# Kernel optimization log

Hardware: AMD Instinct MI355X
Metric: run time of the kernel (lower is better)

Reference implementation:

```python
import jax, jax.numpy as jnp
import numpy as np

WS = 8          # window_size
NH = 8          # num_heads
DIM = 512
INNER = 512
CDIM = 128
CINNER = 128
SHIFTED = True
EPS = 1e-6
N = WS * WS     # tokens per window
SCALE = 1.0 / np.sqrt(INNER // NH + CINNER // NH)  # SDPA scale over fused (feat+coord) head dim


def _rmsnorm(x, g):
    return x * jax.lax.rsqrt(jnp.mean(x * x, axis=-1, keepdims=True) + EPS) * g


def _rel_indices():
    idx = np.array([[x, y] for x in range(WS) for y in range(WS)])
    ri = idx[None, :, :] - idx[:, None, :] + WS - 1
    return ri[..., 0], ri[..., 1]


def _shift_mask(Wh, Ww):
    s = WS
    k = s * (s // 2)
    row = np.zeros((N, N), np.float32)
    row[-k:, :-k] = -np.inf
    row[:-k, -k:] = -np.inf
    col = row.reshape(s, s, s, s).transpose(1, 0, 3, 2).reshape(N, N)
    m = np.zeros((Wh, Ww, N, N), np.float32)
    m[:, -1] += row
    m[-1, :] += col
    return jnp.asarray(m)


def setup_inputs() -> dict:
    key = jax.random.key(0)
    ks = jax.random.split(key, 16)
    B, h, w = 4, 128, 128

    def lin(k, fan_in, fan_out):
        return jax.random.normal(k, (fan_in, fan_out), jnp.float32) * (fan_in ** -0.5)

    return {
        "features": jax.random.normal(ks[0], (B, h, w, DIM), jnp.float32),
        "coords": jax.random.normal(ks[1], (B, h, w, CDIM), jnp.float32),
        "w_fqk": lin(ks[2], DIM, 2 * INNER),
        "b_fqk": jnp.zeros((2 * INNER,), jnp.float32),
        "g_fqk": jnp.ones((2 * INNER,), jnp.float32),
        "w_cqk": lin(ks[3], CDIM, 2 * CINNER),
        "b_cqk": jnp.zeros((2 * CINNER,), jnp.float32),
        "g_cqk": jnp.ones((2 * CINNER,), jnp.float32),
        "w_v": lin(ks[4], DIM, INNER),
        "b_v": jnp.zeros((INNER,), jnp.float32),
        "w_out": lin(ks[5], INNER, DIM),
        "b_out": jnp.zeros((DIM,), jnp.float32),
        "pos_emb": jax.random.normal(ks[6], (2 * WS - 1, 2 * WS - 1), jnp.float32),
    }


def reference(features, coords, w_fqk, b_fqk, g_fqk, w_cqk, b_cqk, g_cqk,
              w_v, b_v, w_out, b_out, pos_emb):
    B, h, w, _ = features.shape
    pad_h = (WS - h % WS) % WS
    pad_w = (WS - w % WS) % WS
    H_pad, W_pad = h + pad_h, w + pad_w
    Wh, Ww = H_pad // WS, W_pad // WS

    fqk = _rmsnorm(features @ w_fqk + b_fqk, g_fqk)
    f_q, f_k = jnp.split(fqk, 2, axis=-1)
    cqk = _rmsnorm(coords @ w_cqk + b_cqk, g_cqk)
    c_q, c_k = jnp.split(cqk, 2, axis=-1)
    f_v = features @ w_v + b_v

    def win(t):
        t = jnp.pad(t, ((0, 0), (0, pad_h), (0, pad_w), (0, 0)))
        if SHIFTED:
            t = jnp.roll(t, (-(WS // 2), -(WS // 2)), axis=(1, 2))
        D = t.shape[-1]
        t = t.reshape(B, Wh, WS, Ww, WS, D).transpose(0, 1, 3, 2, 4, 5)
        return t.reshape(B, Wh, Ww, N, D)

    def heads(t):
        D = t.shape[-1]
        return t.reshape(B, Wh, Ww, N, NH, D // NH)

    fq, fk, fv = heads(win(f_q)), heads(win(f_k)), heads(win(f_v))
    cq, ck = heads(win(c_q)), heads(win(c_k))

    # fused feature + coordinate QK scores, per head per window
    scores = (jnp.einsum('bxyqhd,bxykhd->bxyhqk', fq, fk)
              + jnp.einsum('bxyqhd,bxykhd->bxyhqk', cq, ck)) * SCALE

    ri0, ri1 = _rel_indices()
    pos_bias = pos_emb[ri0, ri1]  # (N, N)
    bias = pos_bias[None, None, None, None]
    if SHIFTED:
        bias = bias + _shift_mask(Wh, Ww)[None, :, :, None]
    scores = scores + bias

    attn = jax.nn.softmax(scores, axis=-1)
    out = jnp.einsum('bxyhqk,bxykhd->bxyqhd', attn, fv)
    out = out.reshape(B, Wh, Ww, N, INNER)

    # un-window
    out = out.reshape(B, Wh, Ww, WS, WS, INNER).transpose(0, 1, 3, 2, 4, 5)
    out = out.reshape(B, H_pad, W_pad, INNER)
    if SHIFTED:
        out = jnp.roll(out, (WS // 2, WS // 2), axis=(1, 2))
    out = out[:, :h, :w, :]
    return out @ w_out + b_out
```

## Files before the change

### kernel.cpp

```cpp
#include <hip/hip_runtime.h>
#include <hip/hip_bf16.h>
#include <type_traits>

using bf16 = __hip_bfloat16;
typedef __bf16 bf16x8 __attribute__((ext_vector_type(8)));
typedef float f32x4 __attribute__((ext_vector_type(4)));

static constexpr int TOKENS = 4 * 128 * 128;
#define SCALE_F 0.11180339887498949f
#define EPS_F 1e-6f

__device__ __forceinline__ float u2f(unsigned short u) {
  union { unsigned int i; float f; } c; c.i = (unsigned int)u << 16; return c.f;
}
__device__ __forceinline__ unsigned short f2u(float f) {
  bf16 h = __float2bfloat16(f); return *reinterpret_cast<unsigned short*>(&h);
}
__device__ __forceinline__ float b2f(bf16 v) { return __bfloat162float(v); }
__device__ __forceinline__ int4 cvt8(const float* p) {
  float4 a = ((const float4*)p)[0], b = ((const float4*)p)[1];
  union { int4 i4; unsigned short s[8]; } u;
  u.s[0] = f2u(a.x); u.s[1] = f2u(a.y); u.s[2] = f2u(a.z); u.s[3] = f2u(a.w);
  u.s[4] = f2u(b.x); u.s[5] = f2u(b.y); u.s[6] = f2u(b.z); u.s[7] = f2u(b.w);
  return u.i4;
}
__device__ __forceinline__ void gload16(const bf16* g, bf16* l) {
  __builtin_amdgcn_global_load_lds(
      (const __attribute__((address_space(1))) unsigned int*)g,
      (__attribute__((address_space(3))) unsigned int*)l, 16, 0, 0);
}

__global__ void convert_k(const float* __restrict__ in, bf16* __restrict__ out,
                          long n) {
  long i = ((long)blockIdx.x * 256 + threadIdx.x) * 8;
  long stride = (long)gridDim.x * 256 * 8;
  for (; i < n; i += stride) *(int4*)(out + i) = cvt8(in + i);
}

__global__ void transpose_k(const float* __restrict__ in, bf16* __restrict__ out,
                            int K, int N) {
  int i = blockIdx.x * 256 + threadIdx.x;
  if (i >= K * N) return;
  int k = i / N, n = i - k * N;
  out[(size_t)n * K + k] = __float2bfloat16(in[i]);
}

__global__ void biascat_k(const float* __restrict__ a, const float* __restrict__ b,
                          float* __restrict__ o) {
  int i = blockIdx.x * 256 + threadIdx.x;
  if (i < 1536) o[i] = i < 1024 ? a[i] : b[i - 1024];
}

template <typename TC, int SSNX>
__global__ __launch_bounds__(256) void gemm128_k(
    const bf16* __restrict__ A, const bf16* __restrict__ Wt,
    const float* __restrict__ bias, TC* __restrict__ C,
    float* __restrict__ ssq, int M, int N, int K) {
  __shared__ __align__(16) bf16 sA[128 * 32];
  __shared__ __align__(16) bf16 sB[128 * 32];
  const int t = threadIdx.x, lane = t & 63, wave = t >> 6;
  const int wr = wave >> 1, wc = wave & 1;
  const int nwg = gridDim.x * gridDim.y;
  int id = blockIdx.y * gridDim.x + blockIdx.x;
  if ((nwg & 7) == 0) id = (id & 7) * (nwg >> 3) + (id >> 3);
  const int bx = id % gridDim.x, by = id / gridDim.x;
  const int bm = by * 128, bn = bx * 128;
  f32x4 acc[4][4] = {};

  const int srow = t >> 2;
  const int ske = (t & 3) * 8;
  bf16* ldsA0 = sA + wave * 512;
  bf16* ldsA1 = sA + 2048 + wave * 512;
  bf16* ldsB0 = sB + wave * 512;
  bf16* ldsB1 = sB + 2048 + wave * 512;
  const int l15 = lane & 15, kg = lane >> 4;
  float bvj[4];
#pragma unroll
  for (int j = 0; j < 4; ++j) bvj[j] = bias[bn + wc * 64 + j * 16 + l15];

  for (int k0 = 0; k0 < K; k0 += 32) {
    gload16(A + (size_t)(bm + srow) * K + k0 + ske, ldsA0);
    gload16(A + (size_t)(bm + 64 + srow) * K + k0 + ske, ldsA1);
    gload16(Wt + (size_t)(bn + srow) * K + k0 + ske, ldsB0);
    gload16(Wt + (size_t)(bn + 64 + srow) * K + k0 + ske, ldsB1);
    __syncthreads();
    bf16x8 af[4], bfr[4];
#pragma unroll
    for (int i = 0; i < 4; ++i) {
      int ar = wr * 64 + i * 16 + l15;
      int br = wc * 64 + i * 16 + l15;
      af[i]  = *(const bf16x8*)(sA + ar * 32 + kg * 8);
      bfr[i] = *(const bf16x8*)(sB + br * 32 + kg * 8);
    }
#pragma unroll
    for (int i = 0; i < 4; ++i)
#pragma unroll
      for (int j = 0; j < 4; ++j)
        acc[i][j] = __builtin_amdgcn_mfma_f32_16x16x32_bf16(af[i], bfr[j], acc[i][j], 0, 0, 0);
    __syncthreads();
  }
#pragma unroll
  for (int i = 0; i < 4; ++i)
#pragma unroll
    for (int j = 0; j < 4; ++j) {
      int col = bn + wc * 64 + j * 16 + l15;
      int rbase = bm + wr * 64 + i * 16 + kg * 4;
#pragma unroll
      for (int r = 0; r < 4; ++r) {
        float val = acc[i][j][r] + bvj[j];
        if constexpr (std::is_same<TC, float>::value)
          C[(size_t)(rbase + r) * N + col] = val;
        else
          C[(size_t)(rbase + r) * N + col] = __float2bfloat16(val);
      }
    }
  if constexpr (SSNX > 0) {
    if (bx < SSNX) {
#pragma unroll
      for (int i = 0; i < 4; ++i) {
        int rbase = bm + wr * 64 + i * 16 + kg * 4;
#pragma unroll
        for (int r = 0; r < 4; ++r) {
          float s = 0.f;
#pragma unroll
          for (int j = 0; j < 4; ++j) {
            float v = acc[i][j][r] + bvj[j];
            s += v * v;
          }
          s += __shfl_xor(s, 1); s += __shfl_xor(s, 2);
          s += __shfl_xor(s, 4); s += __shfl_xor(s, 8);
          if (l15 == 0)
            ssq[(size_t)(rbase + r) * (SSNX * 2) + bx * 2 + wc] = s;
        }
      }
    }
  }
}

__global__ void finalize_rs_k(const float* __restrict__ pf,
                              const float* __restrict__ pc,
                              float* __restrict__ rsf, float* __restrict__ rsc) {
  int i = blockIdx.x * 256 + threadIdx.x;
  if (i >= TOKENS) return;
  float s = 0.f;
#pragma unroll
  for (int j = 0; j < 16; ++j) s += pf[(size_t)i * 16 + j];
  rsf[i] = rsqrtf(s * (1.f / 1024.f) + EPS_F);
  float c = 0.f;
#pragma unroll
  for (int j = 0; j < 4; ++j) c += pc[(size_t)i * 4 + j];
  rsc[i] = rsqrtf(c * (1.f / 256.f) + EPS_F);
}

__global__ __launch_bounds__(256) void attn_mfma_k(
    const bf16* __restrict__ qkv, const bf16* __restrict__ cqk,
    const float* __restrict__ pos, const float* __restrict__ g_fqk,
    const float* __restrict__ g_cqk, const float* __restrict__ rs_f,
    const float* __restrict__ rs_c, bf16* __restrict__ aout) {
  __shared__ __align__(16) bf16 sQ[64][104], sK[64][104];
  __shared__ __align__(16) bf16 sVt[64][72];
  __shared__ __align__(16) bf16 sP[64][72];
  __shared__ float sPos[15][15];
  __shared__ float sRsF[64], sRsC[64];
  const int t = threadIdx.x, lane = t & 63, wave = t >> 6;
  const int head = blockIdx.x & 7;
  const int wid = blockIdx.x >> 3;
  const int wx = wid & 15, wy = (wid >> 4) & 15, b = wid >> 8;

  for (int i = t; i < 225; i += 256) sPos[i / 15][i % 15] = pos[i];
  if (t < 64) {
    const int y = ((wy << 3) + (t >> 3) + 4) & 127;
    const int x = ((wx << 3) + (t & 7) + 4) & 127;
    const size_t tok = ((size_t)b << 14) | (y << 7) | x;
    sRsF[t] = rs_f[tok];
    sRsC[t] = rs_c[tok];
  }
  {
    const int n = t >> 2, p = t & 3;
    const int y = ((wy << 3) + (n >> 3) + 4) & 127;
    const int x = ((wx << 3) + (n & 7) + 4) & 127;
    const size_t tok = ((size_t)b << 14) | (y << 7) | x;
    const bf16* row = qkv + tok * 1536;
    const int4* qp = (const int4*)(row + head * 64 + p * 16);
    ((int4*)&sQ[n][p * 16])[0] = qp[0];
    ((int4*)&sQ[n][p * 16])[1] = qp[1];
    {
      const bf16* kpp = row + 512 + head * 64 + p * 16;
      const float* gq = g_fqk + head * 64 + p * 16;
      const float* gk = g_fqk + 512 + head * 64 + p * 16;
      union { int4 v[2]; unsigned short s[16]; } kt;
#pragma unroll
      for (int i = 0; i < 16; ++i)
        kt.s[i] = f2u(b2f(kpp[i]) * gq[i] * gk[i]);
      ((int4*)&sK[n][p * 16])[0] = kt.v[0];
      ((int4*)&sK[n][p * 16])[1] = kt.v[1];
    }
    const bf16* vp = row + 1024 + head * 64 + p * 16;
#pragma unroll
    for (int i = 0; i < 16; ++i) sVt[p * 16 + i][n] = vp[i];
    const bf16* crow = cqk + tok * 256;
    if (p == 0) {
      const int4* cp = (const int4*)(crow + head * 16);
      ((int4*)&sQ[n][64])[0] = cp[0];
      ((int4*)&sQ[n][64])[1] = cp[1];
    } else if (p == 1) {
      const bf16* ckp = crow + 128 + head * 16;
      const float* gcq = g_cqk + head * 16;
      const float* gck = g_cqk + 128 + head * 16;
      union { int4 v[2]; unsigned short s[16]; } ct;
#pragma unroll
      for (int i = 0; i < 16; ++i)
        ct.s[i] = f2u(b2f(ckp[i]) * gcq[i] * gck[i]);
      ((int4*)&sK[n][64])[0] = ct.v[0];
      ((int4*)&sK[n][64])[1] = ct.v[1];
    } else if (p == 2) {
      ((int4*)&sQ[n][80])[0] = int4{0, 0, 0, 0};
      ((int4*)&sQ[n][80])[1] = int4{0, 0, 0, 0};
    } else {
      ((int4*)&sK[n][80])[0] = int4{0, 0, 0, 0};
      ((int4*)&sK[n][80])[1] = int4{0, 0, 0, 0};
    }
  }
  __syncthreads();

  const int l15 = lane & 15, kg = lane >> 4;
  bf16x8 qa[3];
#pragma unroll
  for (int ko = 0; ko < 3; ++ko)
    qa[ko] = *(const bf16x8*)&sQ[wave * 16 + l15][ko * 32 + kg * 8];
  f32x4 saccf[4] = {}, saccc[4] = {};
#pragma unroll
  for (int j = 0; j < 4; ++j) {
#pragma unroll
    for (int ko = 0; ko < 2; ++ko) {
      bf16x8 kb = *(const bf16x8*)&sK[j * 16 + l15][ko * 32 + kg * 8];
      saccf[j] = __builtin_amdgcn_mfma_f32_16x16x32_bf16(qa[ko], kb, saccf[j], 0, 0, 0);
    }
    bf16x8 kb2 = *(const bf16x8*)&sK[j * 16 + l15][64 + kg * 8];
    saccc[j] = __builtin_amdgcn_mfma_f32_16x16x32_bf16(qa[2], kb2, saccc[j], 0, 0, 0);
  }

  const bool lastx = (wx == 15), lasty = (wy == 15);
  float rqf[4], rqc[4];
#pragma unroll
  for (int r = 0; r < 4; ++r) {
    rqf[r] = sRsF[wave * 16 + kg * 4 + r];
    rqc[r] = sRsC[wave * 16 + kg * 4 + r];
  }
  float sv[4][4], mx[4], sum[4], inv[4];
#pragma unroll
  for (int r = 0; r < 4; ++r) mx[r] = -1e30f;
#pragma unroll
  for (int j = 0; j < 4; ++j) {
    int kcol = j * 16 + l15, kh = kcol >> 3, kw = kcol & 7;
    float rkf = sRsF[kcol], rkc = sRsC[kcol];
#pragma unroll
    for (int r = 0; r < 4; ++r) {
      int q = wave * 16 + kg * 4 + r, qh = q >> 3, qw = q & 7;
      bool msk = (lastx && ((qh >= 4) != (kh >= 4))) ||
                 (lasty && ((qw >= 4) != (kw >= 4)));
      float raw = saccf[j][r] * rqf[r] * rkf + saccc[j][r] * rqc[r] * rkc;
      float val = msk ? -1e30f : raw * SCALE_F + sPos[kh - qh + 7][kw - qw + 7];
      sv[j][r] = val;
      mx[r] = fmaxf(mx[r], val);
    }
  }
#pragma unroll
  for (int m = 1; m < 16; m <<= 1)
#pragma unroll
    for (int r = 0; r < 4; ++r) mx[r] = fmaxf(mx[r], __shfl_xor(mx[r], m));
#pragma unroll
  for (int r = 0; r < 4; ++r) sum[r] = 0.f;
#pragma unroll
  for (int j = 0; j < 4; ++j) {
    int kcol = j * 16 + l15;
#pragma unroll
    for (int r = 0; r < 4; ++r) {
      float e = __expf(sv[j][r] - mx[r]);
      sum[r] += e;
      sP[wave * 16 + kg * 4 + r][kcol] = __float2bfloat16(e);
    }
  }
#pragma unroll
  for (int m = 1; m < 16; m <<= 1)
#pragma unroll
    for (int r = 0; r < 4; ++r) sum[r] += __shfl_xor(sum[r], m);
#pragma unroll
  for (int r = 0; r < 4; ++r) inv[r] = 1.f / sum[r];
  __syncthreads();

  bf16x8 pa[2];
#pragma unroll
  for (int ko = 0; ko < 2; ++ko)
    pa[ko] = *(const bf16x8*)&sP[wave * 16 + l15][ko * 32 + kg * 8];
  f32x4 oacc[4] = {};
#pragma unroll
  for (int jf = 0; jf < 4; ++jf)
#pragma unroll
    for (int ko = 0; ko < 2; ++ko) {
      bf16x8 vb = *(const bf16x8*)&sVt[jf * 16 + l15][ko * 32 + kg * 8];
      oacc[jf] = __builtin_amdgcn_mfma_f32_16x16x32_bf16(pa[ko], vb, oacc[jf], 0, 0, 0);
    }
#pragma unroll
  for (int r = 0; r < 4; ++r) {
    int q = wave * 16 + kg * 4 + r;
    const int y = ((wy << 3) + (q >> 3) + 4) & 127;
    const int x = ((wx << 3) + (q & 7) + 4) & 127;
    const size_t tok = ((size_t)b << 14) | (y << 7) | x;
    bf16* dst = aout + tok * 512 + head * 64;
#pragma unroll
    for (int jf = 0; jf < 4; ++jf)
      dst[jf * 16 + l15] = __float2bfloat16(oacc[jf][r] * inv[r]);
  }
}

extern "C" void kernel_launch(void* const* d_in, const int* in_sizes, int n_in,
                              void* d_out, int out_size, void* d_ws, size_t ws_size,
                              hipStream_t stream) {
  const float* features = (const float*)d_in[0];
  const float* coords   = (const float*)d_in[1];
  const float* w_fqk = (const float*)d_in[2];
  const float* b_fqk = (const float*)d_in[3];
  const float* g_fqk = (const float*)d_in[4];
  const float* w_cqk = (const float*)d_in[5];
  const float* b_cqk = (const float*)d_in[6];
  const float* g_cqk = (const float*)d_in[7];
  const float* w_v   = (const float*)d_in[8];
  const float* b_v   = (const float*)d_in[9];
  const float* w_out = (const float*)d_in[10];
  const float* b_out = (const float*)d_in[11];
  const float* pos_emb = (const float*)d_in[12];
  float* out = (float*)d_out;

  const int M = TOKENS;
  bf16* qkv   = (bf16*)d_ws;
  bf16* cqk   = qkv + (size_t)M * 1536;
  bf16* aout  = cqk + (size_t)M * 256;
  bf16* wcombT = aout + (size_t)M * 512;
  bf16* wcqkT  = wcombT + (size_t)1536 * 512;
  bf16* woutT  = wcqkT + 256 * 128;
  float* bias_comb = (float*)(woutT + 512 * 512);
  float* ssq_f = bias_comb + 1536;
  float* ssq_c = ssq_f + (size_t)M * 16;
  float* rs_f  = ssq_c + (size_t)M * 4;
  float* rs_c  = rs_f + M;
  bf16* fb16 = (bf16*)d_out;
  bf16* cb16 = fb16 + (size_t)M * 512;

  convert_k<<<2048, 256, 0, stream>>>(features, fb16, (long)M * 512);
  convert_k<<<1024, 256, 0, stream>>>(coords, cb16, (long)M * 128);
  transpose_k<<<(512 * 1024 + 255) / 256, 256, 0, stream>>>(w_fqk, wcombT, 512, 1024);
  transpose_k<<<(512 * 512 + 255) / 256, 256, 0, stream>>>(w_v, wcombT + (size_t)1024 * 512, 512, 512);
  transpose_k<<<(128 * 256 + 255) / 256, 256, 0, stream>>>(w_cqk, wcqkT, 128, 256);
  transpose_k<<<(512 * 512 + 255) / 256, 256, 0, stream>>>(w_out, woutT, 512, 512);
  biascat_k<<<6, 256, 0, stream>>>(b_fqk, b_v, bias_comb);

  gemm128_k<bf16, 8><<<dim3(12, 512), 256, 0, stream>>>(fb16, wcombT, bias_comb, qkv, ssq_f, M, 1536, 512);
  gemm128_k<bf16, 2><<<dim3(2, 512), 256, 0, stream>>>(cb16, wcqkT, b_cqk, cqk, ssq_c, M, 256, 128);
  finalize_rs_k<<<TOKENS / 256, 256, 0, stream>>>(ssq_f, ssq_c, rs_f, rs_c);
  attn_mfma_k<<<4 * 16 * 16 * 8, 256, 0, stream>>>(qkv, cqk, pos_emb, g_fqk, g_cqk, rs_f, rs_c, aout);
  gemm128_k<float, 0><<<dim3(4, 512), 256, 0, stream>>>(aout, woutT, b_out, out, nullptr, M, 512, 512);
}
```

Before: 415.4 us.

## Double-buffer GEMM LDS tiles, swizzle LDS layout, transpose MFMA operands for vector stores

```diff
diff --git a/kernel.cpp b/kernel.cpp
--- a/kernel.cpp
+++ b/kernel.cpp
@@ -56,8 +56,8 @@
     const bf16* __restrict__ A, const bf16* __restrict__ Wt,
     const float* __restrict__ bias, TC* __restrict__ C,
     float* __restrict__ ssq, int M, int N, int K) {
-  __shared__ __align__(16) bf16 sA[128 * 32];
-  __shared__ __align__(16) bf16 sB[128 * 32];
+  __shared__ __align__(16) bf16 sA[2][4096];
+  __shared__ __align__(16) bf16 sB[2][4096];
   const int t = threadIdx.x, lane = t & 63, wave = t >> 6;
   const int wr = wave >> 1, wc = wave & 1;
   const int nwg = gridDim.x * gridDim.y;
@@ -65,74 +65,81 @@
   if ((nwg & 7) == 0) id = (id & 7) * (nwg >> 3) + (id >> 3);
   const int bx = id % gridDim.x, by = id / gridDim.x;
   const int bm = by * 128, bn = bx * 128;
+  const int l15 = lane & 15, kg = lane >> 4;
   f32x4 acc[4][4] = {};
 
   const int srow = t >> 2;
-  const int ske = (t & 3) * 8;
-  bf16* ldsA0 = sA + wave * 512;
-  bf16* ldsA1 = sA + 2048 + wave * 512;
-  bf16* ldsB0 = sB + wave * 512;
-  bf16* ldsB1 = sB + 2048 + wave * 512;
-  const int l15 = lane & 15, kg = lane >> 4;
-  float bvj[4];
-#pragma unroll
-  for (int j = 0; j < 4; ++j) bvj[j] = bias[bn + wc * 64 + j * 16 + l15];
-
-  for (int k0 = 0; k0 < K; k0 += 32) {
-    gload16(A + (size_t)(bm + srow) * K + k0 + ske, ldsA0);
-    gload16(A + (size_t)(bm + 64 + srow) * K + k0 + ske, ldsA1);
-    gload16(Wt + (size_t)(bn + srow) * K + k0 + ske, ldsB0);
-    gload16(Wt + (size_t)(bn + 64 + srow) * K + k0 + ske, ldsB1);
+  const int ske = ((t & 3) ^ ((srow >> 1) & 3)) * 8;
+  const bf16* pA0 = A + (size_t)(bm + srow) * K + ske;
+  const bf16* pA1 = A + (size_t)(bm + 64 + srow) * K + ske;
+  const bf16* pB0 = Wt + (size_t)(bn + srow) * K + ske;
+  const bf16* pB1 = Wt + (size_t)(bn + 64 + srow) * K + ske;
+  const int wo = wave * 512;
+
+  gload16(pA0, &sA[0][wo]);
+  gload16(pA1, &sA[0][2048 + wo]);
+  gload16(pB0, &sB[0][wo]);
+  gload16(pB1, &sB[0][2048 + wo]);
+  __syncthreads();
+
+  const int nt = K >> 5;
+  int cur = 0;
+  for (int tt = 0; tt < nt; ++tt) {
+    if (tt + 1 < nt) {
+      pA0 += 32; pA1 += 32; pB0 += 32; pB1 += 32;
+      gload16(pA0, &sA[cur ^ 1][wo]);
+      gload16(pA1, &sA[cur ^ 1][2048 + wo]);
+      gload16(pB0, &sB[cur ^ 1][wo]);
+      gload16(pB1, &sB[cur ^ 1][2048 + wo]);
+    }
+    bf16x8 wf[4], xf[4];
+#pragma unroll
+    for (int i = 0; i < 4; ++i) {
+      int frow = wc * 64 + i * 16 + l15;
+      int xrow = wr * 64 + i * 16 + l15;
+      wf[i] = *(const bf16x8*)(&sB[cur][frow * 32 + ((kg ^ ((frow >> 1) & 3)) * 8)]);
+      xf[i] = *(const bf16x8*)(&sA[cur][xrow * 32 + ((kg ^ ((xrow >> 1) & 3)) * 8)]);
+    }
+#pragma unroll
+    for (int i = 0; i < 4; ++i)
+#pragma unroll
+      for (int j = 0; j < 4; ++j)
+        acc[i][j] = __builtin_amdgcn_mfma_f32_16x16x32_bf16(wf[i], xf[j], acc[i][j], 0, 0, 0);
     __syncthreads();
-    bf16x8 af[4], bfr[4];
+    cur ^= 1;
+  }
+
+  float bvi[4][4];
+#pragma unroll
+  for (int i = 0; i < 4; ++i) {
+    float4 b4 = *(const float4*)(bias + bn + wc * 64 + i * 16 + kg * 4);
+    bvi[i][0] = b4.x; bvi[i][1] = b4.y; bvi[i][2] = b4.z; bvi[i][3] = b4.w;
+  }
+#pragma unroll
+  for (int j = 0; j < 4; ++j) {
+    const int token = bm + wr * 64 + j * 16 + l15;
+    float ssum = 0.f;
 #pragma unroll
     for (int i = 0; i < 4; ++i) {
-      int ar = wr * 64 + i * 16 + l15;
-      int br = wc * 64 + i * 16 + l15;
-      af[i]  = *(const bf16x8*)(sA + ar * 32 + kg * 8);
-      bfr[i] = *(const bf16x8*)(sB + br * 32 + kg * 8);
-    }
-#pragma unroll
-    for (int i = 0; i < 4; ++i)
-#pragma unroll
-      for (int j = 0; j < 4; ++j)
-        acc[i][j] = __builtin_amdgcn_mfma_f32_16x16x32_bf16(af[i], bfr[j], acc[i][j], 0, 0, 0);
-    __syncthreads();
-  }
-#pragma unroll
-  for (int i = 0; i < 4; ++i)
-#pragma unroll
-    for (int j = 0; j < 4; ++j) {
-      int col = bn + wc * 64 + j * 16 + l15;
-      int rbase = bm + wr * 64 + i * 16 + kg * 4;
-#pragma unroll
-      for (int r = 0; r < 4; ++r) {
-        float val = acc[i][j][r] + bvj[j];
-        if constexpr (std::is_same<TC, float>::value)
-          C[(size_t)(rbase + r) * N + col] = val;
-        else
-          C[(size_t)(rbase + r) * N + col] = __float2bfloat16(val);
+      float v0 = acc[i][j][0] + bvi[i][0];
+      float v1 = acc[i][j][1] + bvi[i][1];
+      float v2 = acc[i][j][2] + bvi[i][2];
+      float v3 = acc[i][j][3] + bvi[i][3];
+      const size_t off = (size_t)token * N + bn + wc * 64 + i * 16 + kg * 4;
+      if constexpr (std::is_same<TC, float>::value) {
+        *(float4*)(C + off) = float4{v0, v1, v2, v3};
+      } else {
+        ushort4 pk{f2u(v0), f2u(v1), f2u(v2), f2u(v3)};
+        *(ushort4*)(C + off) = pk;
       }
-    }
-  if constexpr (SSNX > 0) {
-    if (bx < SSNX) {
-#pragma unroll
-      for (int i = 0; i < 4; ++i) {
-        int rbase = bm + wr * 64 + i * 16 + kg * 4;
-#pragma unroll
-        for (int r = 0; r < 4; ++r) {
-          float s = 0.f;
-#pragma unroll
-          for (int j = 0; j < 4; ++j) {
-            float v = acc[i][j][r] + bvj[j];
-            s += v * v;
-          }
-          s += __shfl_xor(s, 1); s += __shfl_xor(s, 2);
-          s += __shfl_xor(s, 4); s += __shfl_xor(s, 8);
-          if (l15 == 0)
-            ssq[(size_t)(rbase + r) * (SSNX * 2) + bx * 2 + wc] = s;
-        }
-      }
+      if constexpr (SSNX > 0)
+        ssum += v0 * v0 + v1 * v1 + v2 * v2 + v3 * v3;
+    }
+    if constexpr (SSNX > 0) {
+      ssum += __shfl_xor(ssum, 16);
+      ssum += __shfl_xor(ssum, 32);
+      if (bx < SSNX && kg == 0)
+        ssq[(size_t)token * (SSNX * 2) + bx * 2 + wc] = ssum;
     }
   }
 }
```

New measurement: 417.2 us. About the same (+0.4%).
